# Kernel tuning notes

Measured on AMD Instinct MI355X. Metric: run time of the kernel, lower is better.

Reference implementation:

```python
import jax, jax.numpy as jnp
import numpy as np
from functools import partial

SAMPLE_RATE = 44100
CUTOFF_HZ = 20.0
# one-pole high-pass coefficient: y[i] = x[i] - x[i-1] + alpha * y[i-1]
ALPHA = float(np.exp(-2.0 * np.pi * CUTOFF_HZ / SAMPLE_RATE))


def setup_inputs() -> dict:
    key = jax.random.key(0)
    k1, k2, k3, k4 = jax.random.split(key, 4)
    B, N = 64, 262144
    return {
        "x": jax.random.normal(k1, (B, N), dtype=jnp.float32),
        "drive": jax.random.uniform(k2, (B, 1), dtype=jnp.float32),
        "bias": jax.random.uniform(k3, (B, 1), dtype=jnp.float32),
        "mix": jax.random.uniform(k4, (B, 1), dtype=jnp.float32),
        "type_idx": 0,
    }


def _waveshape(processed, type_idx):
    if type_idx == 0:
        return jnp.tanh(processed)
    elif type_idx == 1:
        return jnp.clip(processed, -1.0, 1.0)
    elif type_idx == 2:
        return jnp.abs(jnp.remainder(processed + 1.0, 4.0) - 2.0) - 1.0
    elif type_idx == 3:
        return jnp.sin(processed * (np.pi / 2))
    else:
        return processed / (1.0 + jnp.abs(processed))


def _high_pass_filter(x):
    # x: [B, N]; sequential first-order IIR over the time axis via lax.scan
    B = x.shape[0]
    zeros = jnp.zeros((B,), dtype=x.dtype)

    def step(carry, xt):
        last_x, last_y = carry
        yt = xt - last_x + ALPHA * last_y
        return (xt, yt), yt

    _, yT = jax.lax.scan(step, (zeros, zeros), x.T)  # yT: [N, B]
    return yT.T


def reference(x, drive, bias, mix, type_idx):
    drive_gain = jnp.power(10.0, drive * 2.4)
    dc_offset = bias * 2.0 - 1.0
    processed = (x + dc_offset) * drive_gain
    distorted = _waveshape(processed, type_idx)
    distorted = _high_pass_filter(distorted)
    return (1.0 - mix) * x + mix * distorted
```

## Files before the change

kernel.cpp:

```cpp
#include <hip/hip_runtime.h>
#include <math.h>

#define TPB 1024
#define SEG 16
#define HALO 2048
#define BLK (TPB * SEG)
#define CSZ (BLK - HALO)

__device__ __forceinline__ float waveshape(float p, int ty) {
    if (ty == 0) {
        float e2 = __expf(2.0f * p);
        return 1.0f - 2.0f / (e2 + 1.0f);
    } else if (ty == 1) {
        return fminf(fmaxf(p, -1.0f), 1.0f);
    } else if (ty == 2) {
        float r = p + 1.0f;
        float rem = r - 4.0f * floorf(r * 0.25f);
        return fabsf(rem - 2.0f) - 1.0f;
    } else if (ty == 3) {
        return __sinf(p * 1.5707963267948966f);
    } else {
        return p / (1.0f + fabsf(p));
    }
}

__global__ void __launch_bounds__(TPB, 8)
dist_kernel(const float* __restrict__ x,
            const float* __restrict__ drive,
            const float* __restrict__ bias,
            const float* __restrict__ mix,
            const int* __restrict__ type_idx,
            float* __restrict__ out,
            int N, float alpha)
{
    const int row = blockIdx.y;
    const int tid = threadIdx.x;
    const int ty  = *type_idx;

    const float g  = exp2f(drive[row] * 7.972672880099267f);
    const float dc = bias[row] * 2.0f - 1.0f;
    const float mm = mix[row];
    const float om = 1.0f - mm;

    const long long rowBase = (long long)row * (long long)N;
    const float* __restrict__ xr = x + rowBase;
    float* __restrict__ outr = out + rowBase;

    const int outStart = (int)blockIdx.x * CSZ;
    const int j0 = outStart - HALO + tid * SEG;

    float xreg[SEG];
    float d[SEG];
    float e = 0.0f;
    float dprev0;
    {
        int jp = j0 - 1;
        dprev0 = (jp >= 0 && jp < N) ? waveshape((xr[jp] + dc) * g, ty) : 0.0f;
    }
    const bool full = (j0 >= 0) && (j0 + SEG <= N);
    float dprev = dprev0;
    if (full) {
        #pragma unroll
        for (int k = 0; k < SEG; k += 4) {
            float4 xv = *reinterpret_cast<const float4*>(xr + j0 + k);
            xreg[k+0] = xv.x; xreg[k+1] = xv.y; xreg[k+2] = xv.z; xreg[k+3] = xv.w;
        }
        #pragma unroll
        for (int k = 0; k < SEG; ++k) {
            float dv = waveshape((xreg[k] + dc) * g, ty);
            d[k] = dv; e = fmaf(alpha, e, dv - dprev); dprev = dv;
        }
    } else {
        #pragma unroll
        for (int k = 0; k < SEG; ++k) {
            int j = j0 + k;
            bool in = (j >= 0) && (j < N);
            float xs = in ? xr[j] : 0.0f;
            xreg[k] = xs;
            float dv = in ? waveshape((xs + dc) * g, ty) : 0.0f;
            d[k] = dv; e = fmaf(alpha, e, dv - dprev); dprev = dv;
        }
    }

    const int lane = tid & 63;
    const int wv   = tid >> 6;
    float aS = alpha;
    #pragma unroll
    for (int i = 0; i < 4; ++i) aS *= aS;

    float ival = e;
    float m = aS;
    #pragma unroll
    for (int off = 1; off < 64; off <<= 1) {
        float up = __shfl_up(ival, off, 64);
        if (lane >= off) ival = fmaf(m, up, ival);
        m *= m;
    }
    const float aW = m;

    __shared__ float wtot[TPB / 64];
    if (lane == 63) wtot[wv] = ival;
    __syncthreads();

    float P = 0.0f;
    for (int w = 0; w < wv; ++w) P = fmaf(aW, P, wtot[w]);

    float iprev = __shfl_up(ival, 1, 64);
    float ap = 1.0f, b = aS;
    #pragma unroll
    for (int i = 0; i < 6; ++i) { if ((lane >> i) & 1) ap *= b; b *= b; }
    const float carry = fmaf(ap, P, (lane > 0) ? iprev : 0.0f);

    if (tid >= HALO / SEG) {
        float y = carry;
        dprev = dprev0;
        if (full) {
            #pragma unroll
            for (int k = 0; k < SEG; k += 4) {
                float4 ov;
                y = fmaf(alpha, y, d[k+0] - dprev); dprev = d[k+0]; ov.x = fmaf(om, xreg[k+0], mm * y);
                y = fmaf(alpha, y, d[k+1] - dprev); dprev = d[k+1]; ov.y = fmaf(om, xreg[k+1], mm * y);
                y = fmaf(alpha, y, d[k+2] - dprev); dprev = d[k+2]; ov.z = fmaf(om, xreg[k+2], mm * y);
                y = fmaf(alpha, y, d[k+3] - dprev); dprev = d[k+3]; ov.w = fmaf(om, xreg[k+3], mm * y);
                *reinterpret_cast<float4*>(outr + j0 + k) = ov;
            }
        } else {
            #pragma unroll
            for (int k = 0; k < SEG; ++k) {
                int j = j0 + k;
                bool in = (j >= 0) && (j < N);
                y = fmaf(alpha, y, d[k] - dprev); dprev = d[k];
                if (in) outr[j] = fmaf(om, xreg[k], mm * y);
            }
        }
    }
}

extern "C" void kernel_launch(void* const* d_in, const int* in_sizes, int n_in,
                              void* d_out, int out_size, void* d_ws, size_t ws_size,
                              hipStream_t stream) {
    const float* x     = (const float*)d_in[0];
    const float* drive = (const float*)d_in[1];
    const float* bias  = (const float*)d_in[2];
    const float* mixp  = (const float*)d_in[3];
    const int*   tyi   = (const int*)d_in[4];
    float* out = (float*)d_out;

    const int B = in_sizes[1];
    const int N = in_sizes[0] / B;

    const double alpha_d = exp(-2.0 * M_PI * 20.0 / 44100.0);
    const float alpha = (float)alpha_d;

    const int nChunks = (N + CSZ - 1) / CSZ;
    dim3 grid(nChunks, B);
    dist_kernel<<<grid, TPB, 0, stream>>>(x, drive, bias, mixp, tyi, out, N, alpha);
}
```

Before: 136.2 us.

## Reformulate high-pass scan via smoothed state and wave-strided coalesced layout

Rewrites the IIR as a one-pole low-pass state z with y = d - beta*z, which removes the dprev dependency. Each wave now owns a contiguous 1024-sample span split into four 256-wide strided float4 chunks, so memory access is coalesced across lanes. It runs four intra-wave scans in place of one. x is re-read from memory in the output phase rather than kept in registers, which lowers register pressure at the cost of a second read, likely served by cache.

```diff
diff --git a/kernel.cpp b/kernel.cpp
--- a/kernel.cpp
+++ b/kernel.cpp
@@ -2,9 +2,10 @@
 #include <math.h>
 
 #define TPB 1024
-#define SEG 16
+#define WAVES (TPB / 64)
+#define PER_WAVE 1024
+#define BLK (WAVES * PER_WAVE)
 #define HALO 2048
-#define BLK (TPB * SEG)
 #define CSZ (BLK - HALO)
 
 __device__ __forceinline__ float waveshape(float p, int ty) {
@@ -31,11 +32,13 @@
             const float* __restrict__ mix,
             const int* __restrict__ type_idx,
             float* __restrict__ out,
-            int N, float alpha)
+            int N, float alpha, float beta)
 {
-    const int row = blockIdx.y;
-    const int tid = threadIdx.x;
-    const int ty  = *type_idx;
+    const int row  = blockIdx.y;
+    const int tid  = threadIdx.x;
+    const int lane = tid & 63;
+    const int wv   = tid >> 6;
+    const int ty   = *type_idx;
 
     const float g  = exp2f(drive[row] * 7.972672880099267f);
     const float dc = bias[row] * 2.0f - 1.0f;
@@ -47,92 +50,110 @@
     float* __restrict__ outr = out + rowBase;
 
     const int outStart = (int)blockIdx.x * CSZ;
-    const int j0 = outStart - HALO + tid * SEG;
+    const int wbase = outStart - HALO + wv * PER_WAVE;
 
-    float xreg[SEG];
-    float d[SEG];
-    float e = 0.0f;
-    float dprev0;
-    {
-        int jp = j0 - 1;
-        dprev0 = (jp >= 0 && jp < N) ? waveshape((xr[jp] + dc) * g, ty) : 0.0f;
-    }
-    const bool full = (j0 >= 0) && (j0 + SEG <= N);
-    float dprev = dprev0;
-    if (full) {
-        #pragma unroll
-        for (int k = 0; k < SEG; k += 4) {
-            float4 xv = *reinterpret_cast<const float4*>(xr + j0 + k);
-            xreg[k+0] = xv.x; xreg[k+1] = xv.y; xreg[k+2] = xv.z; xreg[k+3] = xv.w;
-        }
-        #pragma unroll
-        for (int k = 0; k < SEG; ++k) {
-            float dv = waveshape((xreg[k] + dc) * g, ty);
-            d[k] = dv; e = fmaf(alpha, e, dv - dprev); dprev = dv;
-        }
-    } else {
-        #pragma unroll
-        for (int k = 0; k < SEG; ++k) {
-            int j = j0 + k;
-            bool in = (j >= 0) && (j < N);
-            float xs = in ? xr[j] : 0.0f;
-            xreg[k] = xs;
-            float dv = in ? waveshape((xs + dc) * g, ty) : 0.0f;
-            d[k] = dv; e = fmaf(alpha, e, dv - dprev); dprev = dv;
+    float4 d4[4];
+    #pragma unroll
+    for (int k = 0; k < 4; ++k) {
+        const int j = wbase + k * 256 + lane * 4;
+        if (j >= 0 && j + 4 <= N) {
+            float4 xv = *reinterpret_cast<const float4*>(xr + j);
+            d4[k].x = waveshape((xv.x + dc) * g, ty);
+            d4[k].y = waveshape((xv.y + dc) * g, ty);
+            d4[k].z = waveshape((xv.z + dc) * g, ty);
+            d4[k].w = waveshape((xv.w + dc) * g, ty);
+        } else {
+            float xs; bool in;
+            in = (j+0 >= 0) && (j+0 < N); xs = in ? xr[j+0] : 0.0f; d4[k].x = in ? waveshape((xs + dc) * g, ty) : 0.0f;
+            in = (j+1 >= 0) && (j+1 < N); xs = in ? xr[j+1] : 0.0f; d4[k].y = in ? waveshape((xs + dc) * g, ty) : 0.0f;
+            in = (j+2 >= 0) && (j+2 < N); xs = in ? xr[j+2] : 0.0f; d4[k].z = in ? waveshape((xs + dc) * g, ty) : 0.0f;
+            in = (j+3 >= 0) && (j+3 < N); xs = in ? xr[j+3] : 0.0f; d4[k].w = in ? waveshape((xs + dc) * g, ty) : 0.0f;
         }
     }
 
-    const int lane = tid & 63;
-    const int wv   = tid >> 6;
-    float aS = alpha;
+    const float a2 = alpha * alpha;
+    const float a4 = a2 * a2;
+    float iv[4];
     #pragma unroll
-    for (int i = 0; i < 4; ++i) aS *= aS;
+    for (int k = 0; k < 4; ++k) {
+        float acc = d4[k].x;
+        acc = fmaf(alpha, acc, d4[k].y);
+        acc = fmaf(alpha, acc, d4[k].z);
+        acc = fmaf(alpha, acc, d4[k].w);
+        iv[k] = acc;
+    }
 
-    float ival = e;
-    float m = aS;
+    float a256;
     #pragma unroll
-    for (int off = 1; off < 64; off <<= 1) {
-        float up = __shfl_up(ival, off, 64);
-        if (lane >= off) ival = fmaf(m, up, ival);
-        m *= m;
+    for (int k = 0; k < 4; ++k) {
+        float v = iv[k];
+        float m = a4;
+        #pragma unroll
+        for (int off = 1; off < 64; off <<= 1) {
+            float up = __shfl_up(v, off, 64);
+            if (lane >= off) v = fmaf(m, up, v);
+            m *= m;
+        }
+        iv[k] = v;
+        a256 = m;
     }
-    const float aW = m;
 
-    __shared__ float wtot[TPB / 64];
-    if (lane == 63) wtot[wv] = ival;
+    float T[4];
+    T[0] = __shfl(iv[0], 63, 64);
+    T[1] = __shfl(iv[1], 63, 64);
+    T[2] = __shfl(iv[2], 63, 64);
+    T[3] = __shfl(iv[3], 63, 64);
+    const float Twave = fmaf(a256, fmaf(a256, fmaf(a256, T[0], T[1]), T[2]), T[3]);
+    const float a1024 = (a256 * a256) * (a256 * a256);
+
+    __shared__ float wtot[WAVES];
+    if (lane == 0) wtot[wv] = Twave;
     __syncthreads();
+    float P = 0.0f;
+    for (int w = 0; w < wv; ++w) P = fmaf(a1024, P, wtot[w]);
 
-    float P = 0.0f;
-    for (int w = 0; w < wv; ++w) P = fmaf(aW, P, wtot[w]);
+    float apl = 1.0f, b = a4;
+    #pragma unroll
+    for (int i = 0; i < 6; ++i) { if ((lane >> i) & 1) apl *= b; b *= b; }
 
-    float iprev = __shfl_up(ival, 1, 64);
-    float ap = 1.0f, b = aS;
+    float S  = 0.0f;
+    float aK = 1.0f;
     #pragma unroll
-    for (int i = 0; i < 6; ++i) { if ((lane >> i) & 1) ap *= b; b *= b; }
-    const float carry = fmaf(ap, P, (lane > 0) ? iprev : 0.0f);
+    for (int k = 0; k < 4; ++k) {
+        const int j = wbase + k * 256 + lane * 4;
+        const float Ck = fmaf(aK, P, S);
+        float ex = __shfl_up(iv[k], 1, 64);
+        if (lane == 0) ex = 0.0f;
+        const float zin = fmaf(apl, Ck, ex);
 
-    if (tid >= HALO / SEG) {
-        float y = carry;
-        dprev = dprev0;
-        if (full) {
-            #pragma unroll
-            for (int k = 0; k < SEG; k += 4) {
-                float4 ov;
-                y = fmaf(alpha, y, d[k+0] - dprev); dprev = d[k+0]; ov.x = fmaf(om, xreg[k+0], mm * y);
-                y = fmaf(alpha, y, d[k+1] - dprev); dprev = d[k+1]; ov.y = fmaf(om, xreg[k+1], mm * y);
-                y = fmaf(alpha, y, d[k+2] - dprev); dprev = d[k+2]; ov.z = fmaf(om, xreg[k+2], mm * y);
-                y = fmaf(alpha, y, d[k+3] - dprev); dprev = d[k+3]; ov.w = fmaf(om, xreg[k+3], mm * y);
-                *reinterpret_cast<float4*>(outr + j0 + k) = ov;
+        if (j >= outStart && j < N) {
+            float4 xv;
+            if (j + 4 <= N) {
+                xv = *reinterpret_cast<const float4*>(xr + j);
+            } else {
+                xv.x = (j + 0 < N) ? xr[j + 0] : 0.0f;
+                xv.y = (j + 1 < N) ? xr[j + 1] : 0.0f;
+                xv.z = (j + 2 < N) ? xr[j + 2] : 0.0f;
+                xv.w = (j + 3 < N) ? xr[j + 3] : 0.0f;
             }
-        } else {
-            #pragma unroll
-            for (int k = 0; k < SEG; ++k) {
-                int j = j0 + k;
-                bool in = (j >= 0) && (j < N);
-                y = fmaf(alpha, y, d[k] - dprev); dprev = d[k];
-                if (in) outr[j] = fmaf(om, xreg[k], mm * y);
+            float z = zin;
+            float4 ov;
+            float y;
+            y = fmaf(-beta, z, d4[k].x); ov.x = fmaf(om, xv.x, mm * y); z = fmaf(alpha, z, d4[k].x);
+            y = fmaf(-beta, z, d4[k].y); ov.y = fmaf(om, xv.y, mm * y); z = fmaf(alpha, z, d4[k].y);
+            y = fmaf(-beta, z, d4[k].z); ov.z = fmaf(om, xv.z, mm * y); z = fmaf(alpha, z, d4[k].z);
+            y = fmaf(-beta, z, d4[k].w); ov.w = fmaf(om, xv.w, mm * y);
+            if (j + 4 <= N) {
+                *reinterpret_cast<float4*>(outr + j) = ov;
+            } else {
+                if (j + 0 < N) outr[j + 0] = ov.x;
+                if (j + 1 < N) outr[j + 1] = ov.y;
+                if (j + 2 < N) outr[j + 2] = ov.z;
+                if (j + 3 < N) outr[j + 3] = ov.w;
             }
         }
+        S  = fmaf(a256, S, T[k]);
+        aK *= a256;
     }
 }
 
@@ -151,8 +172,9 @@
 
     const double alpha_d = exp(-2.0 * M_PI * 20.0 / 44100.0);
     const float alpha = (float)alpha_d;
+    const float beta  = (float)(1.0 - alpha_d);
 
     const int nChunks = (N + CSZ - 1) / CSZ;
     dim3 grid(nChunks, B);
-    dist_kernel<<<grid, TPB, 0, stream>>>(x, drive, bias, mixp, tyi, out, N, alpha);
+    dist_kernel<<<grid, TPB, 0, stream>>>(x, drive, bias, mixp, tyi, out, N, alpha, beta);
 }
```

Result: faster. 129.9 us (-4.6%).
